# Kernel tuning notes

Hardware: AMD Instinct MI355X
Metric: run time of the kernel (lower is better)

## Reference

```python
import jax, jax.numpy as jnp
import numpy as np

D_MODEL, FF_DIM = 1024, 2048
N_SHARED, N_ROUTED, TOP_K = 1, 8, 2
BATCH, SEQ = 2, 2048


def setup_inputs() -> dict:
    key = jax.random.key(0)
    ks = jax.random.split(key, 8)
    init = lambda k, shape: (jax.random.normal(k, shape, jnp.float32) * 0.02)
    x = jax.random.normal(ks[0], (BATCH, SEQ, D_MODEL), jnp.float32)
    Wg = init(ks[1], (D_MODEL, N_ROUTED))                 # gate
    Ws1 = init(ks[2], (D_MODEL, FF_DIM))                  # shared expert (N_SHARED=1)
    Ws3 = init(ks[3], (D_MODEL, FF_DIM))
    Ws2 = init(ks[4], (FF_DIM, D_MODEL))
    We1 = init(ks[5], (N_ROUTED, D_MODEL, FF_DIM))        # routed experts, stacked
    We3 = init(ks[6], (N_ROUTED, D_MODEL, FF_DIM))
    We2 = init(ks[7], (N_ROUTED, FF_DIM, D_MODEL))
    return {"x": x, "Wg": Wg, "Ws1": Ws1, "Ws3": Ws3, "Ws2": Ws2,
            "We1": We1, "We3": We3, "We2": We2}


def reference(x, Wg, Ws1, Ws3, Ws2, We1, We3, We2):
    B, S, d = x.shape
    E = Wg.shape[1]
    xf = x.reshape(-1, d)                                  # [T, d]
    T = xf.shape[0]

    # sigmoid gate + top-k, normalized over selected experts
    gates = jax.nn.sigmoid(xf @ Wg)                        # [T, E]
    vals, idx = jax.lax.top_k(gates, TOP_K)                # [T, K]
    vals = vals / vals.sum(axis=-1, keepdims=True)
    # dense per-expert weights (scatter normalized top-k probs)
    w = jnp.zeros((T, E), x.dtype).at[jnp.arange(T)[:, None], idx].add(vals)  # [T, E]

    # shared expert SwiGLU
    shared = (jax.nn.silu(xf @ Ws1) * (xf @ Ws3)) @ Ws2    # [T, d]

    # routed experts: same math as the torch loop (compute all, mask by w)
    h = jax.nn.silu(jnp.einsum('td,edf->tef', xf, We1)) \
        * jnp.einsum('td,edf->tef', xf, We3)               # [T, E, ff]
    routed = jnp.einsum('tef,efd,te->td', h, We2, w)       # [T, d]

    out = (shared + routed) / (N_SHARED + TOP_K)
    return out.reshape(B, S, d)
```

## Files before the change

### kernel.cpp

```cpp
#include <hip/hip_runtime.h>
#include <stdint.h>

#define TTOK 4096
#define DM   1024
#define FF   2048
#define NE   8

typedef __attribute__((ext_vector_type(8))) short short8;
typedef __attribute__((ext_vector_type(8))) unsigned short ushort8;
typedef __attribute__((ext_vector_type(4))) unsigned short u16x4;
typedef __attribute__((ext_vector_type(4))) float f32x4;

#define OFF_XB      0ull
#define OFF_WB13    (OFF_XB      + (size_t)TTOK*DM*2)
#define OFF_WB2     (OFF_WB13    + (size_t)9*4096*1024*2)
#define OFF_H       (OFF_WB2     + (size_t)9*1024*2048*2)
#define OFF_CONTRIB (OFF_H       + (size_t)12288*2048*2)
#define OFF_TOPKW   (OFF_CONTRIB + (size_t)8192*1024*4)
#define OFF_TOPKI   (OFF_TOPKW   + (size_t)TTOK*2*4)
#define OFF_SLOTTOK (OFF_TOPKI   + (size_t)TTOK*2*4)
#define OFF_TOKSLOT (OFF_SLOTTOK + (size_t)TTOK*2*4)
#define OFF_COUNTS  (OFF_TOKSLOT + (size_t)TTOK*2*4)
#define WS_NEEDED   (OFF_COUNTS + 256)

#define VMWAIT(N) asm volatile("s_waitcnt vmcnt(" #N ")" ::: "memory")
#define LGKM0()   asm volatile("s_waitcnt lgkmcnt(0)" ::: "memory")
#define BAR()     __builtin_amdgcn_s_barrier()
#define SCHED0()  __builtin_amdgcn_sched_barrier(0)

__device__ __forceinline__ unsigned short f2bf(float f) {
  unsigned u = __float_as_uint(f);
  return (unsigned short)((u + 0x7FFFu + ((u >> 16) & 1u)) >> 16);
}
__device__ __forceinline__ float bf2f(unsigned short b) {
  return __uint_as_float((unsigned)b << 16);
}

__device__ __forceinline__ void async16(const void* g, void* l) {
  __builtin_amdgcn_global_load_lds(
      (const __attribute__((address_space(1))) void*)g,
      (__attribute__((address_space(3))) void*)l, 16, 0, 0);
}

__global__ void k_gatecvt(const float* __restrict__ x, const float* __restrict__ Wg,
                          float* __restrict__ topkw, int* __restrict__ topki,
                          unsigned short* __restrict__ xb) {
  int wave = threadIdx.x >> 6;
  int lane = threadIdx.x & 63;
  int t = blockIdx.x * 4 + wave;
  float acc[NE];
#pragma unroll
  for (int e = 0; e < NE; e++) acc[e] = 0.f;
  const float* xr = x + (size_t)t * DM;
  unsigned short* xbr = xb + (size_t)t * DM;
#pragma unroll
  for (int i = 0; i < 4; i++) {
    int k = i * 256 + lane * 4;
    f32x4 xv = *(const f32x4*)(xr + k);
    unsigned short o0 = f2bf(xv[0]), o1 = f2bf(xv[1]), o2 = f2bf(xv[2]), o3 = f2bf(xv[3]);
    unsigned long long pk = (unsigned long long)o0 | ((unsigned long long)o1 << 16) |
                            ((unsigned long long)o2 << 32) | ((unsigned long long)o3 << 48);
    *(unsigned long long*)(xbr + k) = pk;
#pragma unroll
    for (int j = 0; j < 4; j++) {
      const float* wr = Wg + (size_t)(k + j) * NE;
#pragma unroll
      for (int e = 0; e < NE; e++) acc[e] += xv[j] * wr[e];
    }
  }
#pragma unroll
  for (int e = 0; e < NE; e++) {
#pragma unroll
    for (int off = 32; off >= 1; off >>= 1) acc[e] += __shfl_xor(acc[e], off, 64);
  }
  if (lane == 0) {
    float g[NE];
#pragma unroll
    for (int e = 0; e < NE; e++) g[e] = 1.f / (1.f + __expf(-acc[e]));
    int i1 = -1, i2 = -1;
    float m1 = -1e30f, m2 = -1e30f;
#pragma unroll
    for (int e = 0; e < NE; e++) {
      float v = g[e];
      if (v > m1) { m2 = m1; i2 = i1; m1 = v; i1 = e; }
      else if (v > m2) { m2 = v; i2 = e; }
    }
    float s = m1 + m2;
    topkw[t * 2 + 0] = m1 / s;
    topkw[t * 2 + 1] = m2 / s;
    topki[t * 2 + 0] = i1;
    topki[t * 2 + 1] = i2;
  }
}

__global__ void k_route(const int* __restrict__ topki, int* __restrict__ counts_g,
                        int* __restrict__ offs_g, int* __restrict__ slot_token,
                        int* __restrict__ token_slot) {
  __shared__ int cnt[NE], off[NE], fill[NE];
  int tid = threadIdx.x;
  if (tid < NE) { cnt[tid] = 0; fill[tid] = 0; }
  __syncthreads();
  for (int t = tid; t < TTOK; t += 1024) {
    atomicAdd(&cnt[topki[t * 2 + 0]], 1);
    atomicAdd(&cnt[topki[t * 2 + 1]], 1);
  }
  __syncthreads();
  if (tid == 0) {
    int s = 0;
    for (int e = 0; e < NE; e++) { off[e] = s; s += cnt[e]; }
  }
  __syncthreads();
  if (tid < NE) { counts_g[tid] = cnt[tid]; offs_g[tid] = off[tid]; }
  for (int t = tid; t < TTOK; t += 1024) {
#pragma unroll
    for (int k = 0; k < 2; k++) {
      int e = topki[t * 2 + k];
      int pos = atomicAdd(&fill[e], 1);
      int slot = off[e] + pos;
      slot_token[slot] = t;
      token_slot[t * 2 + k] = slot;
    }
  }
}

__global__ void k_tw(const float* __restrict__ We1, const float* __restrict__ We3,
                     const float* __restrict__ Ws1, const float* __restrict__ Ws3,
                     const float* __restrict__ We2, const float* __restrict__ Ws2,
                     unsigned short* __restrict__ wb13, unsigned short* __restrict__ wb2) {
  __shared__ float tile[64][68];
  int bid = blockIdx.x;
  int tid = threadIdx.x;
  int r = tid >> 2, q = tid & 3;
  int nn = tid >> 2, g = tid & 3;

  if (bid < 4608) {
    int z = bid >> 9, rem = bid & 511;
    int by = rem >> 5, bx = rem & 31;
    int r0 = by * 64, c0 = bx * 64;
    unsigned short* dst = wb13 + (size_t)z * 4096 * 1024;
    const float* srcs[2] = {(z < 8) ? We1 + (size_t)z * DM * FF : Ws1,
                            (z < 8) ? We3 + (size_t)z * DM * FF : Ws3};
#pragma unroll
    for (int m = 0; m < 2; m++) {
      const float* src = srcs[m] + (size_t)(r0 + r) * FF + c0;
#pragma unroll
      for (int i = 0; i < 4; i++)
        *(f32x4*)&tile[r][i * 16 + q * 4] = *(const f32x4*)(src + i * 16 + q * 4);
      __syncthreads();
      int n = c0 + nn;
      int d = ((n >> 4) << 5) + (n & 15) + m * 16;
      ushort8 o0, o1;
#pragma unroll
      for (int j = 0; j < 8; j++) o0[j] = f2bf(tile[g * 16 + j][nn]);
#pragma unroll
      for (int j = 0; j < 8; j++) o1[j] = f2bf(tile[g * 16 + 8 + j][nn]);
      unsigned short* dp = dst + (size_t)d * 1024 + r0 + g * 16;
      *(ushort8*)dp = o0;
      *(ushort8*)(dp + 8) = o1;
      __syncthreads();
    }
  } else {
    bid -= 4608;
    int z = bid >> 9, rem = bid & 511;
    int by = rem >> 4, bx = rem & 15;
    int r0 = by * 64, c0 = bx * 64;
    const float* src0 = (z < 8) ? We2 + (size_t)z * FF * DM : Ws2;
    unsigned short* dst = wb2 + (size_t)z * 1024 * 2048;
    const float* src = src0 + (size_t)(r0 + r) * DM + c0;
#pragma unroll
    for (int i = 0; i < 4; i++)
      *(f32x4*)&tile[r][i * 16 + q * 4] = *(const f32x4*)(src + i * 16 + q * 4);
    __syncthreads();
    ushort8 o0, o1;
#pragma unroll
    for (int j = 0; j < 8; j++) o0[j] = f2bf(tile[g * 16 + j][nn]);
#pragma unroll
    for (int j = 0; j < 8; j++) o1[j] = f2bf(tile[g * 16 + 8 + j][nn]);
    unsigned short* dp = dst + (size_t)(c0 + nn) * 2048 + r0 + g * 16;
    *(ushort8*)dp = o0;
    *(ushort8*)(dp + 8) = o1;
  }
}

template <bool G13, int K, int NBROW>
__global__ __launch_bounds__(512, 2) void k_gemm(
    const unsigned short* __restrict__ A, const unsigned short* __restrict__ B,
    unsigned short* __restrict__ Hout, unsigned short* __restrict__ Cout,
    float* __restrict__ Dout,
    const int* __restrict__ slot_token, const int* __restrict__ offs,
    const int* __restrict__ counts) {
  __shared__ unsigned short lds[2][2][2][8192];
  const int NT = K / 64;

  int e = blockIdx.z;
  int seg, cnt;
  if (e == 8) { seg = 8192; cnt = 4096; }
  else        { seg = offs[e]; cnt = counts[e]; }
  int m0 = blockIdx.y * 256;
  if (m0 >= cnt) return;
  int bn = blockIdx.x;

  int tid = threadIdx.x, lane = tid & 63, w = tid >> 6;

  int srcslot = (((tid & 7) ^ ((tid >> 3) & 7)) << 4);
  const char* aptr[2][2];
  const char* bptr[2][2];
#pragma unroll
  for (int half = 0; half < 2; half++)
#pragma unroll
    for (int j = 0; j < 2; j++) {
      int rl = half * 128 + j * 64 + (tid >> 3);
      int r = m0 + rl; if (r > cnt - 1) r = cnt - 1;
      long tok;
      if (G13) tok = (e == 8) ? (long)r : (long)slot_token[seg + r];
      else     tok = (long)(seg + r);
      aptr[half][j] = (const char*)A + ((size_t)tok * K) * 2 + srcslot;
      int br = bn * 256 + rl;
      bptr[half][j] = (const char*)B + (((size_t)e * NBROW + br) * K) * 2 + srcslot;
    }

#define STG(b, op, half, kt) do {                                           \
    const char* _p0 = (op ? bptr : aptr)[half][0] + (size_t)(kt) * 128;     \
    const char* _p1 = (op ? bptr : aptr)[half][1] + (size_t)(kt) * 128;     \
    async16(_p0, &lds[b][op][half][(size_t)w * 512]);                       \
    async16(_p1, &lds[b][op][half][4096 + (size_t)w * 512]);                \
  } while (0)

  int wr = w >> 2, wc = w & 3, wch = wc >> 1;
  int s0 = (((0 + (lane >> 4)) ^ (lane & 7)) << 4);
  int s1 = (((4 + (lane >> 4)) ^ (lane & 7)) << 4);

  f32x4 acc[8][4];
#pragma unroll
  for (int i = 0; i < 8; i++)
#pragma unroll
    for (int j = 0; j < 4; j++) acc[i][j] = (f32x4){0.f, 0.f, 0.f, 0.f};

  short8 Af[2][2], Bf[4][2];

#define DO_PHASE(LA, LB, qq, STG_STMT, WAIT_STMT) do {                        \
    if (qq == 0) {                                                            \
      _Pragma("unroll") for (int nf = 0; nf < 4; nf++) {                      \
        int rb = ((wc & 1) * 64 + nf * 16 + (lane & 15)) * 128;               \
        Bf[nf][0] = *(const short8*)((LB) + rb + s0);                         \
        Bf[nf][1] = *(const short8*)((LB) + rb + s1);                         \
      }                                                                       \
    }                                                                         \
    _Pragma("unroll") for (int m2 = 0; m2 < 2; m2++) {                        \
      int ra = (((qq) * 2 + m2) * 16 + (lane & 15)) * 128;                    \
      Af[m2][0] = *(const short8*)((LA) + ra + s0);                           \
      Af[m2][1] = *(const short8*)((LA) + ra + s1);                           \
    }                                                                         \
    STG_STMT;                                                                 \
    BAR();                                                                    \
    LGKM0();                                                                  \
    SCHED0();                                                                 \
    __builtin_amdgcn_s_setprio(1);                                            \
    _Pragma("unroll") for (int m2 = 0; m2 < 2; m2++)                          \
      _Pragma("unroll") for (int nf = 0; nf < 4; nf++) {                      \
        acc[(qq) * 2 + m2][nf] = __builtin_amdgcn_mfma_f32_16x16x32_bf16(     \
            Af[m2][0], Bf[nf][0], acc[(qq) * 2 + m2][nf], 0, 0, 0);           \
        acc[(qq) * 2 + m2][nf] = __builtin_amdgcn_mfma_f32_16x16x32_bf16(     \
            Af[m2][1], Bf[nf][1], acc[(qq) * 2 + m2][nf], 0, 0, 0);           \
      }                                                                       \
    __builtin_amdgcn_s_setprio(0);                                            \
    WAIT_STMT;                                                                \
    BAR();                                                                    \
  } while (0)

  STG(0, 1, 0, 0);
  STG(0, 1, 1, 0);
  STG(0, 0, 0, 0);
  STG(0, 0, 1, 0);
  STG(1, 1, 0, 1);
  VMWAIT(2);
  BAR();

  const char* LA0 = (const char*)&lds[0][0][wr][0];
  const char* LB0 = (const char*)&lds[0][1][wch][0];
  const char* LA1 = (const char*)&lds[1][0][wr][0];
  const char* LB1 = (const char*)&lds[1][1][wch][0];

  for (int it = 0; it < NT / 2; ++it) {
    int t1 = 2 * it + 1;
    int n2 = (2 * it + 2 < NT) ? 2 * it + 2 : NT - 1;
    int n3 = (2 * it + 3 < NT) ? 2 * it + 3 : NT - 1;
    DO_PHASE(LA0, LB0, 0, STG(1, 1, 1, t1), );
    DO_PHASE(LA0, LB0, 1, STG(1, 0, 0, t1), );
    DO_PHASE(LA0, LB0, 2, STG(1, 0, 1, t1), );
    DO_PHASE(LA0, LB0, 3, STG(0, 1, 0, n2), VMWAIT(2));
    DO_PHASE(LA1, LB1, 0, STG(0, 1, 1, n2), );
    DO_PHASE(LA1, LB1, 1, STG(0, 0, 0, n2), );
    DO_PHASE(LA1, LB1, 2, STG(0, 0, 1, n2), );
    DO_PHASE(LA1, LB1, 3, STG(1, 1, 0, n3), VMWAIT(2));
  }
  VMWAIT(0);
#undef DO_PHASE
#undef STG

  if (G13) {
#pragma unroll
    for (int mi = 0; mi < 8; mi++)
#pragma unroll
      for (int j = 0; j < 2; j++)
#pragma unroll
        for (int q = 0; q < 4; q++) {
          int rl = wr * 128 + mi * 16 + (lane >> 4) * 4 + q;
          if (m0 + rl < cnt) {
            float s1v = acc[mi][2 * j][q], s3v = acc[mi][2 * j + 1][q];
            float h = (s1v / (1.f + __expf(-s1v))) * s3v;
            int ffcol = (bn * 8 + wc * 2 + j) * 16 + (lane & 15);
            Hout[(size_t)(seg + m0 + rl) * 2048 + ffcol] = f2bf(h);
          }
        }
  } else {
#pragma unroll
    for (int mi = 0; mi < 8; mi++)
#pragma unroll
      for (int nf = 0; nf < 4; nf++)
#pragma unroll
        for (int q = 0; q < 4; q++) {
          int rl = wr * 128 + mi * 16 + (lane >> 4) * 4 + q;
          if (m0 + rl < cnt) {
            int col = bn * 256 + wc * 64 + nf * 16 + (lane & 15);
            if (e == 8) Dout[(size_t)(m0 + rl) * 1024 + col] = acc[mi][nf][q];
            else        Cout[(size_t)(seg + m0 + rl) * 1024 + col] = f2bf(acc[mi][nf][q]);
          }
        }
  }
}

__global__ void k_combine(float* __restrict__ out, const unsigned short* __restrict__ contrib,
                          const int* __restrict__ token_slot, const float* __restrict__ topkw) {
  int t = blockIdx.x;
  int c = threadIdx.x * 4;
  int s0 = token_slot[t * 2 + 0], s1 = token_slot[t * 2 + 1];
  float w0 = topkw[t * 2 + 0], w1 = topkw[t * 2 + 1];
  float* po = out + (size_t)t * DM + c;
  const unsigned short* p0 = contrib + (size_t)s0 * DM + c;
  const unsigned short* p1 = contrib + (size_t)s1 * DM + c;
  f32x4 vo = *(f32x4*)po;
  u16x4 v0 = *(const u16x4*)p0;
  u16x4 v1 = *(const u16x4*)p1;
#pragma unroll
  for (int i = 0; i < 4; i++)
    vo[i] = (vo[i] + w0 * bf2f(v0[i]) + w1 * bf2f(v1[i])) * (1.f / 3.f);
  *(f32x4*)po = vo;
}

extern "C" void kernel_launch(void* const* d_in, const int* in_sizes, int n_in,
                              void* d_out, int out_size, void* d_ws, size_t ws_size,
                              hipStream_t stream) {
  const float* x   = (const float*)d_in[0];
  const float* Wg  = (const float*)d_in[1];
  const float* Ws1 = (const float*)d_in[2];
  const float* Ws3 = (const float*)d_in[3];
  const float* Ws2 = (const float*)d_in[4];
  const float* We1 = (const float*)d_in[5];
  const float* We3 = (const float*)d_in[6];
  const float* We2 = (const float*)d_in[7];
  float* out = (float*)d_out;

  if (ws_size < WS_NEEDED) return;

  char* w = (char*)d_ws;
  unsigned short* xb      = (unsigned short*)(w + OFF_XB);
  unsigned short* wb13    = (unsigned short*)(w + OFF_WB13);
  unsigned short* wb2     = (unsigned short*)(w + OFF_WB2);
  unsigned short* H       = (unsigned short*)(w + OFF_H);
  unsigned short* contrib = (unsigned short*)(w + OFF_CONTRIB);
  float* topkw            = (float*)(w + OFF_TOPKW);
  int* topki              = (int*)(w + OFF_TOPKI);
  int* slot_token         = (int*)(w + OFF_SLOTTOK);
  int* token_slot         = (int*)(w + OFF_TOKSLOT);
  int* counts             = (int*)(w + OFF_COUNTS);
  int* offs               = counts + 16;

  k_gatecvt<<<TTOK / 4, 256, 0, stream>>>(x, Wg, topkw, topki, xb);
  k_route<<<1, 1024, 0, stream>>>(topki, counts, offs, slot_token, token_slot);
  k_tw<<<9216, 256, 0, stream>>>(We1, We3, Ws1, Ws3, We2, Ws2, wb13, wb2);

  k_gemm<true, 1024, 4096><<<dim3(16, 16, 9), 512, 0, stream>>>(
      xb, wb13, H, nullptr, nullptr, slot_token, offs, counts);
  k_gemm<false, 2048, 1024><<<dim3(4, 16, 9), 512, 0, stream>>>(
      H, wb2, nullptr, contrib, out, slot_token, offs, counts);

  k_combine<<<TTOK, 256, 0, stream>>>(out, contrib, token_slot, topkw);
}
```

Measured before the change: 319.0 us.

## Split-K the down-projection GEMM four ways and reduce partials in combine

The second GEMM (H times W2) is split along K into four slices via blockIdx.z, which quadruples the grid so more CUs stay busy on a small-M problem. Each slice writes bf16 partials: three go into the now-dead wb13 buffer, one into contrib. The shared-expert output also moves to bf16 partials instead of fp32 written straight to out. The combine kernel then sums the shared and both routed partials across all four slices. This adds extra partial-store and reload traffic, and adds rounding error because the shared expert is now stored in bf16.

```diff
diff --git a/kernel.cpp b/kernel.cpp
--- a/kernel.cpp
+++ b/kernel.cpp
@@ -23,6 +23,8 @@
 #define OFF_COUNTS  (OFF_TOKSLOT + (size_t)TTOK*2*4)
 #define WS_NEEDED   (OFF_COUNTS + 256)
 
+#define PARTROWS    ((size_t)12288 * 1024)
+
 #define VMWAIT(N) asm volatile("s_waitcnt vmcnt(" #N ")" ::: "memory")
 #define LGKM0()   asm volatile("s_waitcnt lgkmcnt(0)" ::: "memory")
 #define BAR()     __builtin_amdgcn_s_barrier()
@@ -182,17 +184,19 @@
   }
 }
 
-template <bool G13, int K, int NBROW>
+template <bool G13, int K, int KSP, int NBROW>
 __global__ __launch_bounds__(512, 2) void k_gemm(
     const unsigned short* __restrict__ A, const unsigned short* __restrict__ B,
     unsigned short* __restrict__ Hout, unsigned short* __restrict__ Cout,
-    float* __restrict__ Dout,
+    unsigned short* __restrict__ Pw,
     const int* __restrict__ slot_token, const int* __restrict__ offs,
     const int* __restrict__ counts) {
   __shared__ unsigned short lds[2][2][2][8192];
-  const int NT = K / 64;
-
-  int e = blockIdx.z;
+  const int NTL = K / 64 / KSP;
+
+  int zz = blockIdx.z;
+  int e = zz % 9, ks = zz / 9;
+  const int KB = ks * NTL;
   int seg, cnt;
   if (e == 8) { seg = 8192; cnt = 4096; }
   else        { seg = offs[e]; cnt = counts[e]; }
@@ -219,11 +223,11 @@
       bptr[half][j] = (const char*)B + (((size_t)e * NBROW + br) * K) * 2 + srcslot;
     }
 
-#define STG(b, op, half, kt) do {                                           \
-    const char* _p0 = (op ? bptr : aptr)[half][0] + (size_t)(kt) * 128;     \
-    const char* _p1 = (op ? bptr : aptr)[half][1] + (size_t)(kt) * 128;     \
-    async16(_p0, &lds[b][op][half][(size_t)w * 512]);                       \
-    async16(_p1, &lds[b][op][half][4096 + (size_t)w * 512]);                \
+#define STG(b, op, half, kt) do {                                                \
+    const char* _p0 = (op ? bptr : aptr)[half][0] + (size_t)(KB + (kt)) * 128;   \
+    const char* _p1 = (op ? bptr : aptr)[half][1] + (size_t)(KB + (kt)) * 128;   \
+    async16(_p0, &lds[b][op][half][(size_t)w * 512]);                            \
+    async16(_p1, &lds[b][op][half][4096 + (size_t)w * 512]);                     \
   } while (0)
 
   int wr = w >> 2, wc = w & 3, wch = wc >> 1;
@@ -281,10 +285,10 @@
   const char* LA1 = (const char*)&lds[1][0][wr][0];
   const char* LB1 = (const char*)&lds[1][1][wch][0];
 
-  for (int it = 0; it < NT / 2; ++it) {
+  for (int it = 0; it < NTL / 2; ++it) {
     int t1 = 2 * it + 1;
-    int n2 = (2 * it + 2 < NT) ? 2 * it + 2 : NT - 1;
-    int n3 = (2 * it + 3 < NT) ? 2 * it + 3 : NT - 1;
+    int n2 = (2 * it + 2 < NTL) ? 2 * it + 2 : NTL - 1;
+    int n3 = (2 * it + 3 < NTL) ? 2 * it + 3 : NTL - 1;
     DO_PHASE(LA0, LB0, 0, STG(1, 1, 1, t1), );
     DO_PHASE(LA0, LB0, 1, STG(1, 0, 0, t1), );
     DO_PHASE(LA0, LB0, 2, STG(1, 0, 1, t1), );
@@ -314,6 +318,7 @@
           }
         }
   } else {
+    unsigned short* Cp = (ks < 3) ? (Pw + (size_t)ks * PARTROWS) : Cout;
 #pragma unroll
     for (int mi = 0; mi < 8; mi++)
 #pragma unroll
@@ -323,29 +328,34 @@
           int rl = wr * 128 + mi * 16 + (lane >> 4) * 4 + q;
           if (m0 + rl < cnt) {
             int col = bn * 256 + wc * 64 + nf * 16 + (lane & 15);
-            if (e == 8) Dout[(size_t)(m0 + rl) * 1024 + col] = acc[mi][nf][q];
-            else        Cout[(size_t)(seg + m0 + rl) * 1024 + col] = f2bf(acc[mi][nf][q]);
+            Cp[(size_t)(seg + m0 + rl) * 1024 + col] = f2bf(acc[mi][nf][q]);
           }
         }
   }
 }
 
-__global__ void k_combine(float* __restrict__ out, const unsigned short* __restrict__ contrib,
+__global__ void k_combine(float* __restrict__ out, const unsigned short* __restrict__ PW,
+                          const unsigned short* __restrict__ PC,
                           const int* __restrict__ token_slot, const float* __restrict__ topkw) {
   int t = blockIdx.x;
   int c = threadIdx.x * 4;
   int s0 = token_slot[t * 2 + 0], s1 = token_slot[t * 2 + 1];
   float w0 = topkw[t * 2 + 0], w1 = topkw[t * 2 + 1];
+  f32x4 sum = (f32x4){0.f, 0.f, 0.f, 0.f};
+#pragma unroll
+  for (int ks = 0; ks < 4; ks++) {
+    const unsigned short* P = (ks < 3) ? (PW + (size_t)ks * PARTROWS) : PC;
+    u16x4 vs = *(const u16x4*)(P + (size_t)(8192 + t) * DM + c);
+    u16x4 v0 = *(const u16x4*)(P + (size_t)s0 * DM + c);
+    u16x4 v1 = *(const u16x4*)(P + (size_t)s1 * DM + c);
+#pragma unroll
+    for (int i = 0; i < 4; i++)
+      sum[i] += bf2f(vs[i]) + w0 * bf2f(v0[i]) + w1 * bf2f(v1[i]);
+  }
   float* po = out + (size_t)t * DM + c;
-  const unsigned short* p0 = contrib + (size_t)s0 * DM + c;
-  const unsigned short* p1 = contrib + (size_t)s1 * DM + c;
-  f32x4 vo = *(f32x4*)po;
-  u16x4 v0 = *(const u16x4*)p0;
-  u16x4 v1 = *(const u16x4*)p1;
-#pragma unroll
-  for (int i = 0; i < 4; i++)
-    vo[i] = (vo[i] + w0 * bf2f(v0[i]) + w1 * bf2f(v1[i])) * (1.f / 3.f);
-  *(f32x4*)po = vo;
+#pragma unroll
+  for (int i = 0; i < 4; i++) sum[i] *= (1.f / 3.f);
+  *(f32x4*)po = sum;
 }
 
 extern "C" void kernel_launch(void* const* d_in, const int* in_sizes, int n_in,
@@ -380,10 +390,10 @@
   k_route<<<1, 1024, 0, stream>>>(topki, counts, offs, slot_token, token_slot);
   k_tw<<<9216, 256, 0, stream>>>(We1, We3, Ws1, Ws3, We2, Ws2, wb13, wb2);
 
-  k_gemm<true, 1024, 4096><<<dim3(16, 16, 9), 512, 0, stream>>>(
+  k_gemm<true, 1024, 1, 4096><<<dim3(16, 16, 9), 512, 0, stream>>>(
       xb, wb13, H, nullptr, nullptr, slot_token, offs, counts);
-  k_gemm<false, 2048, 1024><<<dim3(4, 16, 9), 512, 0, stream>>>(
-      H, wb2, nullptr, contrib, out, slot_token, offs, counts);
-
-  k_combine<<<TTOK, 256, 0, stream>>>(out, contrib, token_slot, topkw);
-}
+  k_gemm<false, 2048, 4, 1024><<<dim3(4, 16, 36), 512, 0, stream>>>(
+      H, wb2, nullptr, contrib, wb13, slot_token, offs, counts);
+
+  k_combine<<<TTOK, 256, 0, stream>>>(out, wb13, contrib, token_slot, topkw);
+}
```

Result: no change. 316.1 us (-0.9%).
